# Kernel tuning notes

Hardware: AMD Instinct MI355X
Metric: run time of the kernel (lower is better)

## Reference

```python
import jax, jax.numpy as jnp
import numpy as np

EMB = 384
HEAD_DIM = 64  # emb_size / num_head = 384 / 6
B, S = 8, 2048


def setup_inputs() -> dict:
    key = jax.random.key(0)
    k1, k2, k3, k4 = jax.random.split(key, 4)
    x = jax.random.normal(k1, (B, S, EMB), dtype=jnp.float32)
    # nn.Linear(emb, head_dim, bias=False): store as [in, out] so q = x @ W
    scale = 0.02
    Wq = jax.random.normal(k2, (EMB, HEAD_DIM), dtype=jnp.float32) * scale
    Wk = jax.random.normal(k3, (EMB, HEAD_DIM), dtype=jnp.float32) * scale
    Wv = jax.random.normal(k4, (EMB, HEAD_DIM), dtype=jnp.float32) * scale
    return {"x": x, "Wq": Wq, "Wk": Wk, "Wv": Wv}


def reference(x, Wq, Wk, Wv):
    # x: [B, S, C]
    q = jnp.einsum('bsc,cd->bsd', x, Wq)  # [B,S,D]
    k = jnp.einsum('bsc,cd->bsd', x, Wk)
    v = jnp.einsum('bsc,cd->bsd', x, Wv)
    scores = jnp.einsum('bid,bjd->bij', q, k) * (HEAD_DIM ** -0.5)  # [B,S,S]
    # causal mask: positions with tril==0 (j > i) set to -inf
    causal = jnp.tril(jnp.ones((S, S), dtype=bool))  # [S,S]
    scores = jnp.where(causal[None, :, :], scores, -jnp.inf)
    # NOTE: faithful to original — softmax over dim=1 (query axis), not -1.
    attn = jax.nn.softmax(scores, axis=1)  # [B,S,S]
    out = jnp.einsum('bij,bjd->bid', attn, v)  # [B,S,D]
    return out
```

## Files before the change

kernel.cpp:

```cpp
#include <hip/hip_runtime.h>
#include <hip/hip_bf16.h>
#include <math.h>

#define B_N 8
#define S_N 2048
#define C_N 384
#define D_N 64
#define NPART 4
#define NEG_BIG (-1e30f)

typedef __bf16 bf16x8 __attribute__((ext_vector_type(8)));
typedef float f32x4 __attribute__((ext_vector_type(4)));

static __device__ __forceinline__ bf16x8 ldfrag(const __bf16* p) {
  return *reinterpret_cast<const bf16x8*>(p);
}

static __device__ __forceinline__ void gload16(void* lds, const void* gsrc) {
  __builtin_amdgcn_global_load_lds(
      (const __attribute__((address_space(1))) unsigned int*)gsrc,
      (__attribute__((address_space(3))) unsigned int*)lds, 16, 0, 0);
}

__global__ __launch_bounds__(256) void w_prep(
    const float* __restrict__ Wq, const float* __restrict__ Wk,
    const float* __restrict__ Wv, __bf16* __restrict__ Wt) {
  const int idx = blockIdx.x * 256 + threadIdx.x;
  const int m = idx / (64 * C_N);
  const int r = idx % (64 * C_N);
  const int d = r / C_N;
  const int c = r % C_N;
  const float* W = (m == 0) ? Wq : (m == 1) ? Wk : Wv;
  Wt[idx] = (__bf16)W[c * 64 + d];
}

__global__ __launch_bounds__(384) void qkv_mfma(
    const float* __restrict__ x, const __bf16* __restrict__ Wt,
    __bf16* __restrict__ Q, __bf16* __restrict__ K, __bf16* __restrict__ Vt) {
  const int t = threadIdx.x;
  const int w = t >> 6, lane = t & 63, lr = lane & 15, lg = lane >> 4;
  const int mat = w >> 1, rh = w & 1;
  const int row0 = blockIdx.x * 32;
  const int ri = row0 + rh * 16 + lr;

  __shared__ __bf16 vtile[32][66];

  const float scl = (mat == 0) ? 0.125f : 1.0f;
  const float* xr = x + (size_t)ri * C_N;
  const __bf16* Wm = Wt + (size_t)mat * 64 * C_N;

  f32x4 acc[4];
#pragma unroll
  for (int nt = 0; nt < 4; ++nt) acc[nt] = {0.f, 0.f, 0.f, 0.f};

  float4 xa = *reinterpret_cast<const float4*>(xr + lg * 8);
  float4 xb = *reinterpret_cast<const float4*>(xr + lg * 8 + 4);
  bf16x8 bw[4];
#pragma unroll
  for (int nt = 0; nt < 4; ++nt)
    bw[nt] = ldfrag(Wm + (size_t)(nt * 16 + lr) * C_N + lg * 8);

  for (int kk = 0; kk < C_N / 32; ++kk) {
    const int kn = (kk + 1 < C_N / 32) ? kk + 1 : kk;
    const float4 xan = *reinterpret_cast<const float4*>(xr + kn * 32 + lg * 8);
    const float4 xbn = *reinterpret_cast<const float4*>(xr + kn * 32 + lg * 8 + 4);
    bf16x8 bwn[4];
#pragma unroll
    for (int nt = 0; nt < 4; ++nt)
      bwn[nt] = ldfrag(Wm + (size_t)(nt * 16 + lr) * C_N + kn * 32 + lg * 8);

    bf16x8 a;
    a[0] = (__bf16)(xa.x * scl); a[1] = (__bf16)(xa.y * scl);
    a[2] = (__bf16)(xa.z * scl); a[3] = (__bf16)(xa.w * scl);
    a[4] = (__bf16)(xb.x * scl); a[5] = (__bf16)(xb.y * scl);
    a[6] = (__bf16)(xb.z * scl); a[7] = (__bf16)(xb.w * scl);
#pragma unroll
    for (int nt = 0; nt < 4; ++nt)
      acc[nt] = __builtin_amdgcn_mfma_f32_16x16x32_bf16(a, bw[nt], acc[nt], 0, 0, 0);

    xa = xan; xb = xbn;
#pragma unroll
    for (int nt = 0; nt < 4; ++nt) bw[nt] = bwn[nt];
  }

  if (mat < 2) {
    __bf16* outp = (mat == 0) ? Q : K;
#pragma unroll
    for (int nt = 0; nt < 4; ++nt)
#pragma unroll
      for (int r = 0; r < 4; ++r)
        outp[(size_t)(row0 + rh * 16 + lg * 4 + r) * 64 + nt * 16 + lr] =
            (__bf16)acc[nt][r];
  } else {
#pragma unroll
    for (int nt = 0; nt < 4; ++nt)
#pragma unroll
      for (int r = 0; r < 4; ++r)
        vtile[rh * 16 + lg * 4 + r][nt * 16 + lr] = (__bf16)acc[nt][r];
  }
  __syncthreads();

  const int b = row0 >> 11, s0 = row0 & (S_N - 1);
  for (int idx = t; idx < 64 * 32; idx += 384) {
    const int d = idx >> 5, s2 = idx & 31;
    Vt[((size_t)b * D_N + d) * S_N + s0 + s2] = vtile[s2][d];
  }
}

__global__ __launch_bounds__(512) void col_stats(
    const __bf16* __restrict__ Q, const __bf16* __restrict__ K,
    float* __restrict__ zpart) {
  const int wg = blockIdx.x;
  const int b  = wg & 7;
  const int jb = (wg >> 3) & 15;
  const int h  = wg >> 7;
  const int j0 = jb * 128;

  const int t = threadIdx.x;
  const int q = t >> 6;
  const int lane = t & 63, lr = lane & 15, lg = lane >> 4;

  const int n = 32 - 2 * jb;
  const int itStart = 2 * jb + (n * h) / NPART;
  const int itEnd   = 2 * jb + (n * (h + 1)) / NPART;
  float* zout = zpart + (size_t)h * B_N * S_N + (size_t)b * S_N;

  if (itStart >= itEnd) {
    if (lg == 0) zout[j0 + q * 16 + lr] = 0.f;
    return;
  }

  __shared__ __align__(16) __bf16 QT[2][64][64];

  const __bf16* Qb = Q + (size_t)b * S_N * 64;
  const __bf16* Kb = K + (size_t)b * S_N * 64;

  const int jg = j0 + q * 16 + lr;
  const bf16x8 bk0 = ldfrag(Kb + (size_t)jg * 64 + lg * 8);
  const bf16x8 bk1 = ldfrag(Kb + (size_t)jg * 64 + 32 + lg * 8);

  const int r0 = t >> 3, c0 = t & 7;
  const int gq = c0 ^ (r0 & 7);

#define STAGE_Q(BUF, TILE) \
  gload16(&QT[BUF][r0][c0 * 8], Qb + (size_t)((TILE) * 64 + r0) * 64 + gq * 8)

  STAGE_Q(0, itStart);
  __syncthreads();

  float z = 0.f;
  int cur = 0;
  for (int it = itStart; it < itEnd; ++it) {
    const int i0 = it * 64;
    if (it + 1 < itEnd) STAGE_Q(cur ^ 1, it + 1);

#pragma unroll
    for (int s = 0; s < 4; ++s) {
      const int arow = s * 16 + lr;
      const bf16x8 aq0 = ldfrag(&QT[cur][arow][(lg ^ (arow & 7)) * 8]);
      const bf16x8 aq1 = ldfrag(&QT[cur][arow][((4 + lg) ^ (arow & 7)) * 8]);
      f32x4 s4 = {0.f, 0.f, 0.f, 0.f};
      s4 = __builtin_amdgcn_mfma_f32_16x16x32_bf16(aq0, bk0, s4, 0, 0, 0);
      s4 = __builtin_amdgcn_mfma_f32_16x16x32_bf16(aq1, bk1, s4, 0, 0, 0);
      const int ibase = i0 + s * 16 + lg * 4;
      float es = 0.f;
#pragma unroll
      for (int r = 0; r < 4; ++r)
        es += (ibase + r >= jg) ? __expf(s4[r]) : 0.f;
      es += __shfl_xor(es, 16);
      es += __shfl_xor(es, 32);
      z += es;
    }

    __syncthreads();
    cur ^= 1;
  }
#undef STAGE_Q

  if (lg == 0) zout[jg] = z;
}

__global__ __launch_bounds__(512) void attn_out(
    const __bf16* __restrict__ Q, const __bf16* __restrict__ K,
    const __bf16* __restrict__ Vt, const float* __restrict__ zpart,
    float* __restrict__ opart) {
  const int wg = blockIdx.x;
  const int b  = wg & 7;
  const int ib = (wg >> 3) & 15;
  const int h  = wg >> 7;

  const int t = threadIdx.x;
  const int s = t >> 6;
  const int lane = t & 63, lr = lane & 15, lg = lane >> 4;
  const int i0 = ib * 128;

  const int n = 2 * ib + 2;
  const int jbStart = (n * h) / NPART;
  const int jbEnd   = (n * (h + 1)) / NPART;

  float* op = opart + (size_t)h * B_N * S_N * D_N + (size_t)b * S_N * D_N;
  const int ibase = i0 + s * 16 + lg * 4;

  f32x4 o[4];
#pragma unroll
  for (int dt = 0; dt < 4; ++dt) o[dt] = {0.f, 0.f, 0.f, 0.f};

  if (jbStart < jbEnd) {
    __shared__ __align__(16) __bf16 KT[2][64][64];
    __shared__ __align__(16) __bf16 VT[2][64][64];
    __shared__ __align__(16) __bf16 P[8][16][72];

    const __bf16* Qb  = Q  + (size_t)b * S_N * 64;
    const __bf16* Kb  = K  + (size_t)b * S_N * 64;
    const __bf16* Vtb = Vt + (size_t)b * D_N * S_N;
    const float*  zp  = zpart + (size_t)b * S_N;

    const int r0 = t >> 3, c0 = t & 7;
    const int gq = c0 ^ (r0 & 7);

#define STAGE_KV(BUF, TJ0) do { \
      gload16(&KT[BUF][r0][c0 * 8], Kb + (size_t)((TJ0) + r0) * 64 + gq * 8); \
      gload16(&VT[BUF][r0][c0 * 8], Vtb + (size_t)r0 * S_N + (TJ0) + gq * 8); \
    } while (0)

    const int ri = i0 + s * 16 + lr;
    const bf16x8 aq0 = ldfrag(Qb + (size_t)ri * 64 + lg * 8);
    const bf16x8 aq1 = ldfrag(Qb + (size_t)ri * 64 + 32 + lg * 8);

    STAGE_KV(0, jbStart * 64);
    __syncthreads();

    int cur = 0;
    for (int jb = jbStart; jb < jbEnd; ++jb) {
      const int j0 = jb * 64;
      if (jb + 1 < jbEnd) STAGE_KV(cur ^ 1, j0 + 64);

#pragma unroll
      for (int jt = 0; jt < 4; ++jt) {
        const int krow = jt * 16 + lr;
        const bf16x8 bk0 = ldfrag(&KT[cur][krow][(lg ^ (krow & 7)) * 8]);
        const bf16x8 bk1 = ldfrag(&KT[cur][krow][((4 + lg) ^ (krow & 7)) * 8]);
        f32x4 s4 = {0.f, 0.f, 0.f, 0.f};
        s4 = __builtin_amdgcn_mfma_f32_16x16x32_bf16(aq0, bk0, s4, 0, 0, 0);
        s4 = __builtin_amdgcn_mfma_f32_16x16x32_bf16(aq1, bk1, s4, 0, 0, 0);
        const int jg = j0 + jt * 16 + lr;
        const float rz = 1.0f / (zp[jg] + zp[(size_t)B_N * S_N + jg] +
                                 zp[(size_t)2 * B_N * S_N + jg] +
                                 zp[(size_t)3 * B_N * S_N + jg]);
#pragma unroll
        for (int r = 0; r < 4; ++r) {
          const float pv = (jg <= ibase + r) ? __expf(s4[r]) * rz : 0.f;
          P[s][lg * 4 + r][jt * 16 + lr] = (__bf16)pv;
        }
      }

      const bf16x8 ap0 = ldfrag(&P[s][lr][lg * 8]);
      const bf16x8 ap1 = ldfrag(&P[s][lr][32 + lg * 8]);
#pragma unroll
      for (int dt = 0; dt < 4; ++dt) {
        const int vrow = dt * 16 + lr;
        const bf16x8 bv0 = ldfrag(&VT[cur][vrow][(lg ^ (vrow & 7)) * 8]);
        const bf16x8 bv1 = ldfrag(&VT[cur][vrow][((4 + lg) ^ (vrow & 7)) * 8]);
        o[dt] = __builtin_amdgcn_mfma_f32_16x16x32_bf16(ap0, bv0, o[dt], 0, 0, 0);
        o[dt] = __builtin_amdgcn_mfma_f32_16x16x32_bf16(ap1, bv1, o[dt], 0, 0, 0);
      }

      __syncthreads();
      cur ^= 1;
    }
#undef STAGE_KV
  }

#pragma unroll
  for (int dt = 0; dt < 4; ++dt)
#pragma unroll
    for (int r = 0; r < 4; ++r)
      op[(size_t)(ibase + r) * D_N + dt * 16 + lr] = o[dt][r];
}

__global__ __launch_bounds__(256) void combine(
    const float* __restrict__ opart, float* __restrict__ out) {
  const size_t idx = (size_t)blockIdx.x * 256 + threadIdx.x;
  const size_t stride = (size_t)B_N * S_N * D_N;
  out[idx] = opart[idx] + opart[stride + idx] + opart[2 * stride + idx] +
             opart[3 * stride + idx];
}

extern "C" void kernel_launch(void* const* d_in, const int* in_sizes, int n_in,
                              void* d_out, int out_size, void* d_ws, size_t ws_size,
                              hipStream_t stream) {
  (void)in_sizes; (void)n_in; (void)ws_size; (void)out_size;
  const float* x  = (const float*)d_in[0];
  const float* Wq = (const float*)d_in[1];
  const float* Wk = (const float*)d_in[2];
  const float* Wv = (const float*)d_in[3];
  float* out = (float*)d_out;

  __bf16* Qb = (__bf16*)d_ws;
  __bf16* Kb = Qb + (size_t)B_N * S_N * D_N;
  __bf16* Vt = Kb + (size_t)B_N * S_N * D_N;
  float* zpart = (float*)(Vt + (size_t)B_N * S_N * D_N);
  float* opart = zpart + (size_t)NPART * B_N * S_N;
  __bf16* Wt = (__bf16*)(opart + (size_t)NPART * B_N * S_N * D_N);

  w_prep<<<dim3(3 * 64 * C_N / 256), dim3(256), 0, stream>>>(Wq, Wk, Wv, Wt);
  qkv_mfma<<<dim3(B_N * S_N / 32), dim3(384), 0, stream>>>(x, Wt, Qb, Kb, Vt);
  col_stats<<<dim3(NPART * 16 * B_N), dim3(512), 0, stream>>>(Qb, Kb, zpart);
  attn_out<<<dim3(NPART * 16 * B_N), dim3(512), 0, stream>>>(Qb, Kb, Vt, zpart, opart);
  combine<<<dim3(B_N * S_N * D_N / 256), dim3(256), 0, stream>>>(opart, out);
}
```

Measured before the change: 75.78 us.

## Pre-convert x to bf16 in prep kernel and shrink QKV projection tiles

The weight-prep kernel becomes a combined prep kernel that also converts x from fp32 to a bf16 buffer and folds the Q scale into Wq. The QKV projection then reads bf16 x directly and uses 16-row blocks with each wave computing half the output columns, doubling the grid size. The aim is to cut the redundant fp32 x loads and per-wave conversion, which were repeated across the three matrices, and to raise parallelism. The cost is an extra full pass writing and re-reading a bf16 copy of x through global memory.

```diff
diff --git a/kernel.cpp b/kernel.cpp
--- a/kernel.cpp
+++ b/kernel.cpp
@@ -22,87 +22,86 @@
       (__attribute__((address_space(3))) unsigned int*)lds, 16, 0, 0);
 }
 
-__global__ __launch_bounds__(256) void w_prep(
+__global__ __launch_bounds__(256) void prep(
+    const float* __restrict__ x,
     const float* __restrict__ Wq, const float* __restrict__ Wk,
-    const float* __restrict__ Wv, __bf16* __restrict__ Wt) {
-  const int idx = blockIdx.x * 256 + threadIdx.x;
-  const int m = idx / (64 * C_N);
-  const int r = idx % (64 * C_N);
-  const int d = r / C_N;
-  const int c = r % C_N;
-  const float* W = (m == 0) ? Wq : (m == 1) ? Wk : Wv;
-  Wt[idx] = (__bf16)W[c * 64 + d];
+    const float* __restrict__ Wv,
+    __bf16* __restrict__ xb, __bf16* __restrict__ Wt) {
+  const int blk = blockIdx.x;
+  if (blk < 36) {
+    const int idx = blk * 2048 + threadIdx.x * 8;
+    const int m = idx / (64 * C_N);
+    const int r = idx % (64 * C_N);
+    const int d = r / C_N;
+    const int c = r % C_N;
+    const float* W = (m == 0) ? Wq : (m == 1) ? Wk : Wv;
+    const float s = (m == 0) ? 0.125f : 1.0f;
+    bf16x8 v;
+#pragma unroll
+    for (int i = 0; i < 8; ++i) v[i] = (__bf16)(W[(c + i) * 64 + d] * s);
+    *reinterpret_cast<bf16x8*>(Wt + idx) = v;
+  } else {
+    const size_t idx = (size_t)(blk - 36) * 2048 + (size_t)threadIdx.x * 8;
+    const float4 a = *reinterpret_cast<const float4*>(x + idx);
+    const float4 b = *reinterpret_cast<const float4*>(x + idx + 4);
+    bf16x8 v;
+    v[0] = (__bf16)a.x; v[1] = (__bf16)a.y; v[2] = (__bf16)a.z; v[3] = (__bf16)a.w;
+    v[4] = (__bf16)b.x; v[5] = (__bf16)b.y; v[6] = (__bf16)b.z; v[7] = (__bf16)b.w;
+    *reinterpret_cast<bf16x8*>(xb + idx) = v;
+  }
 }
 
 __global__ __launch_bounds__(384) void qkv_mfma(
-    const float* __restrict__ x, const __bf16* __restrict__ Wt,
+    const __bf16* __restrict__ xb, const __bf16* __restrict__ Wt,
     __bf16* __restrict__ Q, __bf16* __restrict__ K, __bf16* __restrict__ Vt) {
   const int t = threadIdx.x;
   const int w = t >> 6, lane = t & 63, lr = lane & 15, lg = lane >> 4;
-  const int mat = w >> 1, rh = w & 1;
-  const int row0 = blockIdx.x * 32;
-  const int ri = row0 + rh * 16 + lr;
-
-  __shared__ __bf16 vtile[32][66];
-
-  const float scl = (mat == 0) ? 0.125f : 1.0f;
-  const float* xr = x + (size_t)ri * C_N;
+  const int mat = w >> 1, nh = w & 1;
+  const int row0 = blockIdx.x * 16;
+
+  __shared__ __bf16 vtile[16][68];
+
+  const __bf16* xr = xb + (size_t)(row0 + lr) * C_N;
   const __bf16* Wm = Wt + (size_t)mat * 64 * C_N;
 
-  f32x4 acc[4];
-#pragma unroll
-  for (int nt = 0; nt < 4; ++nt) acc[nt] = {0.f, 0.f, 0.f, 0.f};
-
-  float4 xa = *reinterpret_cast<const float4*>(xr + lg * 8);
-  float4 xb = *reinterpret_cast<const float4*>(xr + lg * 8 + 4);
-  bf16x8 bw[4];
-#pragma unroll
-  for (int nt = 0; nt < 4; ++nt)
-    bw[nt] = ldfrag(Wm + (size_t)(nt * 16 + lr) * C_N + lg * 8);
+  f32x4 acc0 = {0.f, 0.f, 0.f, 0.f};
+  f32x4 acc1 = {0.f, 0.f, 0.f, 0.f};
+
+  bf16x8 a   = ldfrag(xr + lg * 8);
+  bf16x8 bw0 = ldfrag(Wm + (size_t)(nh * 32 + lr) * C_N + lg * 8);
+  bf16x8 bw1 = ldfrag(Wm + (size_t)(nh * 32 + 16 + lr) * C_N + lg * 8);
 
   for (int kk = 0; kk < C_N / 32; ++kk) {
     const int kn = (kk + 1 < C_N / 32) ? kk + 1 : kk;
-    const float4 xan = *reinterpret_cast<const float4*>(xr + kn * 32 + lg * 8);
-    const float4 xbn = *reinterpret_cast<const float4*>(xr + kn * 32 + lg * 8 + 4);
-    bf16x8 bwn[4];
-#pragma unroll
-    for (int nt = 0; nt < 4; ++nt)
-      bwn[nt] = ldfrag(Wm + (size_t)(nt * 16 + lr) * C_N + kn * 32 + lg * 8);
-
-    bf16x8 a;
-    a[0] = (__bf16)(xa.x * scl); a[1] = (__bf16)(xa.y * scl);
-    a[2] = (__bf16)(xa.z * scl); a[3] = (__bf16)(xa.w * scl);
-    a[4] = (__bf16)(xb.x * scl); a[5] = (__bf16)(xb.y * scl);
-    a[6] = (__bf16)(xb.z * scl); a[7] = (__bf16)(xb.w * scl);
-#pragma unroll
-    for (int nt = 0; nt < 4; ++nt)
-      acc[nt] = __builtin_amdgcn_mfma_f32_16x16x32_bf16(a, bw[nt], acc[nt], 0, 0, 0);
-
-    xa = xan; xb = xbn;
-#pragma unroll
-    for (int nt = 0; nt < 4; ++nt) bw[nt] = bwn[nt];
+    const bf16x8 an   = ldfrag(xr + kn * 32 + lg * 8);
+    const bf16x8 b0n  = ldfrag(Wm + (size_t)(nh * 32 + lr) * C_N + kn * 32 + lg * 8);
+    const bf16x8 b1n  = ldfrag(Wm + (size_t)(nh * 32 + 16 + lr) * C_N + kn * 32 + lg * 8);
+
+    acc0 = __builtin_amdgcn_mfma_f32_16x16x32_bf16(a, bw0, acc0, 0, 0, 0);
+    acc1 = __builtin_amdgcn_mfma_f32_16x16x32_bf16(a, bw1, acc1, 0, 0, 0);
+
+    a = an; bw0 = b0n; bw1 = b1n;
   }
 
   if (mat < 2) {
     __bf16* outp = (mat == 0) ? Q : K;
 #pragma unroll
-    for (int nt = 0; nt < 4; ++nt)
-#pragma unroll
-      for (int r = 0; r < 4; ++r)
-        outp[(size_t)(row0 + rh * 16 + lg * 4 + r) * 64 + nt * 16 + lr] =
-            (__bf16)acc[nt][r];
+    for (int r = 0; r < 4; ++r) {
+      outp[(size_t)(row0 + lg * 4 + r) * 64 + nh * 32 + lr] = (__bf16)acc0[r];
+      outp[(size_t)(row0 + lg * 4 + r) * 64 + nh * 32 + 16 + lr] = (__bf16)acc1[r];
+    }
   } else {
 #pragma unroll
-    for (int nt = 0; nt < 4; ++nt)
-#pragma unroll
-      for (int r = 0; r < 4; ++r)
-        vtile[rh * 16 + lg * 4 + r][nt * 16 + lr] = (__bf16)acc[nt][r];
+    for (int r = 0; r < 4; ++r) {
+      vtile[lg * 4 + r][nh * 32 + lr] = (__bf16)acc0[r];
+      vtile[lg * 4 + r][nh * 32 + 16 + lr] = (__bf16)acc1[r];
+    }
   }
   __syncthreads();
 
   const int b = row0 >> 11, s0 = row0 & (S_N - 1);
-  for (int idx = t; idx < 64 * 32; idx += 384) {
-    const int d = idx >> 5, s2 = idx & 31;
+  for (int idx = t; idx < 64 * 16; idx += 384) {
+    const int d = idx >> 4, s2 = idx & 15;
     Vt[((size_t)b * D_N + d) * S_N + s0 + s2] = vtile[s2][d];
   }
 }
@@ -302,9 +301,11 @@
   float* zpart = (float*)(Vt + (size_t)B_N * S_N * D_N);
   float* opart = zpart + (size_t)NPART * B_N * S_N;
   __bf16* Wt = (__bf16*)(opart + (size_t)NPART * B_N * S_N * D_N);
-
-  w_prep<<<dim3(3 * 64 * C_N / 256), dim3(256), 0, stream>>>(Wq, Wk, Wv, Wt);
-  qkv_mfma<<<dim3(B_N * S_N / 32), dim3(384), 0, stream>>>(x, Wt, Qb, Kb, Vt);
+  __bf16* xbuf = Wt + (size_t)3 * 64 * C_N;
+
+  prep<<<dim3(36 + B_N * S_N * C_N / 2048), dim3(256), 0, stream>>>(
+      x, Wq, Wk, Wv, xbuf, Wt);
+  qkv_mfma<<<dim3(B_N * S_N / 16), dim3(384), 0, stream>>>(xbuf, Wt, Qb, Kb, Vt);
   col_stats<<<dim3(NPART * 16 * B_N), dim3(512), 0, stream>>>(Qb, Kb, zpart);
   attn_out<<<dim3(NPART * 16 * B_N), dim3(512), 0, stream>>>(Qb, Kb, Vt, zpart, opart);
   combine<<<dim3(B_N * S_N * D_N / 256), dim3(256), 0, stream>>>(opart, out);
```

After: 77.63 us. 1.02x slower.
